# Kernel optimization log

Measured on AMD Instinct MI355X. Metric: run time of the kernel, lower is better.

Reference implementation:

```python
import jax, jax.numpy as jnp
import numpy as np

EPS = 1e-5
B, NPB, G = 8, 12500, 64
N = B * NPB
N_EMB, NI, NF = 256, 128, 64
C = NI // 2  # 64


def _bn_relu(x, g, b):
    m = jnp.mean(x, axis=0)
    v = jnp.mean((x - m) ** 2, axis=0)
    return jax.nn.relu(g * (x - m) * jax.lax.rsqrt(v + EPS) + b)


def setup_inputs() -> dict:
    rng = np.random.default_rng(0)
    # unique voxel coords per batch in a 64^3 grid
    coords = np.concatenate([
        np.stack(np.unravel_index(rng.choice(G ** 3, NPB, replace=False), (G, G, G)), axis=1)
        for _ in range(B)
    ], axis=0).astype(np.int64)  # [N,3]
    batch_idx = np.repeat(np.arange(B), NPB).astype(np.int64)
    keys = ((batch_idx * G + coords[:, 0]) * G + coords[:, 1]) * G + coords[:, 2]
    order = np.argsort(keys)
    skeys = keys[order]
    offs = np.array([[dx, dy, dz] for dx in (-1, 0, 1) for dy in (-1, 0, 1) for dz in (-1, 0, 1)], np.int64)
    nbr = np.full((27, N), -1, np.int32)  # rulebook: input idx feeding each output per offset
    for k in range(27):
        nc = coords + offs[k]
        inb = np.all((nc >= 0) & (nc < G), axis=1)
        q = ((batch_idx * G + nc[:, 0]) * G + nc[:, 1]) * G + nc[:, 2]
        pos = np.clip(np.searchsorted(skeys, q), 0, N - 1)
        hit = inb & (skeys[pos] == q)
        nbr[k] = np.where(hit, order[pos], -1).astype(np.int32)

    key = jax.random.key(0)
    ks = jax.random.split(key, 8)
    s1 = 1.0 / np.sqrt(NI)
    s3 = 1.0 / np.sqrt(27 * C)
    su = 1.0 / np.sqrt(C)
    st = 1.0 / np.sqrt(N_EMB)
    return {
        "feats": jax.random.normal(ks[0], (N, NI), jnp.float32),
        "t": jax.random.normal(ks[1], (B, N_EMB), jnp.float32),
        "w_fuse": jax.random.normal(ks[2], (NI, C), jnp.float32) * s1,
        "g1": jnp.ones((C,), jnp.float32), "b1": jnp.zeros((C,), jnp.float32),
        "w_temb": jax.random.normal(ks[3], (N_EMB, C), jnp.float32) * st,
        "b_temb": jnp.zeros((C,), jnp.float32),
        "w3": jax.random.normal(ks[4], (27, C, C), jnp.float32) * s3,
        "g2": jnp.ones((C,), jnp.float32), "b2": jnp.zeros((C,), jnp.float32),
        "wup": jax.random.normal(ks[5], (8, C, NF), jnp.float32) * su,
        "g3": jnp.ones((NF,), jnp.float32), "b3": jnp.zeros((NF,), jnp.float32),
        "batch_idx": jnp.asarray(batch_idx, jnp.int32),
        "nbr": jnp.asarray(nbr),
    }


def reference(feats, t, w_fuse, g1, b1, w_temb, b_temb, w3, g2, b2, wup, g3, b3, batch_idx, nbr):
    # feature_fusion: 1x1 sparse conv == per-point GEMM, then BN + ReLU
    h = _bn_relu(feats @ w_fuse, g1, b1)  # [N, C]
    # time embedding injected per point via batch index
    emb = jax.nn.silu(t) @ w_temb + b_temb  # [B, C]
    h = h + emb[batch_idx]
    # 3x3x3 submanifold sparse conv: gather-GEMM-scatter per kernel offset
    n = h.shape[0]
    out = jnp.zeros_like(h)
    for k in range(nbr.shape[0]):  # fixed 27 offsets
        idx = nbr[k]
        valid = (idx >= 0)[:, None]
        g_k = jnp.where(valid, h[jnp.clip(idx, 0, n - 1)], 0.0)
        out = out + g_k @ w3[k]
    h2 = _bn_relu(out, g2, b2)  # [N, C]
    # transposed conv k=2 s=2: each input spawns 8 unique children -> per-offset GEMM
    up = jnp.einsum('nc,kcf->nkf', h2, wup).reshape(n * wup.shape[0], wup.shape[2])  # [8N, NF]
    return _bn_relu(up, g3, b3)
```

## Files before the change

### kernel.cpp

```cpp
#include <hip/hip_runtime.h>

#define EPSV 1e-5f

typedef __attribute__((ext_vector_type(8))) short short8;
typedef __attribute__((ext_vector_type(4))) short s16x4;
typedef __attribute__((ext_vector_type(4))) float f32x4;
typedef unsigned short ushort_t;

__device__ inline ushort_t f2bf(float f) {
    unsigned int x = __builtin_bit_cast(unsigned int, f);
    unsigned int r = (x + 0x7fffu + ((x >> 16) & 1u)) >> 16;
    return (ushort_t)r;
}
__device__ inline float bf2f(ushort_t u) {
    return __builtin_bit_cast(float, (unsigned int)u << 16);
}

__global__ __launch_bounds__(256) void k_prep(
    const float* __restrict__ w_fuse, const float* __restrict__ w3,
    const float* __restrict__ wup,
    const float* __restrict__ tin, const float* __restrict__ w_temb,
    const float* __restrict__ b_temb, float* __restrict__ emb,
    ushort_t* __restrict__ wfuset2, ushort_t* __restrict__ w3t2,
    ushort_t* __restrict__ wupt, ushort_t* __restrict__ wupt2) {
    if (blockIdx.x == 720) {
        __shared__ float st[8 * 256];
        int t = threadIdx.x;
        for (int i = t; i < 2048; i += 256) { float v = tin[i]; st[i] = v / (1.f + __expf(-v)); }
        __syncthreads();
        for (int p = t; p < 512; p += 256) {
            int bb = p >> 6, c = p & 63;
            float acc = b_temb[c];
            for (int e = 0; e < 256; e++) acc += st[bb * 256 + e] * w_temb[e * 64 + c];
            emb[bb * 64 + c] = acc;
        }
        return;
    }
    int i = blockIdx.x * 256 + threadIdx.x;
    if (i < 8192) {
        int kk = i & 127, ln = (i >> 7) & 15, j = i >> 11;
        wfuset2[i] = f2bf(w_fuse[kk * 64 + 4 * ln + j]);
    } else if (i < 118784) {
        int p = i - 8192;
        int kk = p & 63, ln = (p >> 6) & 15, j = (p >> 10) & 3, k = p >> 12;
        w3t2[p] = f2bf(w3[k * 4096 + kk * 64 + 4 * ln + j]);
    } else if (i < 151552) {
        int p = i - 118784;
        int uk = p >> 12, r = p & 4095, f = r >> 6, c = r & 63;
        wupt[p] = f2bf(wup[uk * 4096 + c * 64 + f]);
    } else if (i < 184320) {
        int p = i - 151552;
        int kk = p & 63, ln = (p >> 6) & 15, j = (p >> 10) & 3, uk = p >> 12;
        wupt2[p] = f2bf(wup[uk * 4096 + kk * 64 + 4 * ln + j]);
    }
}

__global__ __launch_bounds__(256) void k_gemm_fuse(
    const float* __restrict__ feats, const ushort_t* __restrict__ wfuset2,
    ushort_t* __restrict__ T, float* __restrict__ partialT, int npts) {
    __shared__ float sm[4][128];
    int t = threadIdx.x, bid = blockIdx.x;
    int lane = t & 63, w = t >> 6, q = lane >> 4, ln = lane & 15;
    int rbase = bid * 64 + w * 16;
    int row = rbase + ln;
    bool rv = row < npts;
    short8 afr[4];
#pragma unroll
    for (int s = 0; s < 4; s++) {
        short8 v = (short8)0;
        if (rv) {
            const float* src = feats + (size_t)row * 128 + s * 32 + q * 8;
            float4 a = *(const float4*)src;
            float4 b = *(const float4*)(src + 4);
            ushort_t u[8] = {f2bf(a.x), f2bf(a.y), f2bf(a.z), f2bf(a.w),
                             f2bf(b.x), f2bf(b.y), f2bf(b.z), f2bf(b.w)};
            v = *(short8*)u;
        }
        afr[s] = v;
    }
    f32x4 acc[4];
#pragma unroll
    for (int j = 0; j < 4; j++) acc[j] = (f32x4)0.f;
#pragma unroll
    for (int s = 0; s < 4; s++)
#pragma unroll
        for (int j = 0; j < 4; j++) {
            short8 bfr = *(const short8*)&wfuset2[j * 2048 + ln * 128 + s * 32 + q * 8];
            acc[j] = __builtin_amdgcn_mfma_f32_16x16x32_bf16(afr[s], bfr, acc[j], 0, 0, 0);
        }
    float ps[4] = {0, 0, 0, 0}, pq[4] = {0, 0, 0, 0};
#pragma unroll
    for (int r = 0; r < 4; r++) {
        int rr = rbase + q * 4 + r;
        ushort_t o[4];
#pragma unroll
        for (int j = 0; j < 4; j++) {
            float v = acc[j][r];
            ps[j] += v; pq[j] += v * v;
            o[j] = f2bf(v);
        }
        if (rr < npts) *(s16x4*)&T[(size_t)rr * 64 + 4 * ln] = *(s16x4*)o;
    }
#pragma unroll
    for (int j = 0; j < 4; j++) {
        ps[j] += __shfl_xor(ps[j], 16); ps[j] += __shfl_xor(ps[j], 32);
        pq[j] += __shfl_xor(pq[j], 16); pq[j] += __shfl_xor(pq[j], 32);
    }
    if (lane < 16) {
#pragma unroll
        for (int j = 0; j < 4; j++) {
            sm[w][ln * 4 + j] = ps[j];
            sm[w][64 + ln * 4 + j] = pq[j];
        }
    }
    __syncthreads();
    if (t < 128)
        partialT[(size_t)t * 2048 + bid] = sm[0][t] + sm[1][t] + sm[2][t] + sm[3][t];
}

__global__ __launch_bounds__(256) void k_finalize(
    const float* __restrict__ partialT, int nrows, float inv_count,
    const float* __restrict__ g, const float* __restrict__ b, float* __restrict__ prm) {
    int c = blockIdx.x;
    int t = threadIdx.x;
    float S = 0.f, Q = 0.f;
    for (int r = t; r < nrows; r += 256) {
        S += partialT[(size_t)c * 2048 + r];
        Q += partialT[(size_t)(64 + c) * 2048 + r];
    }
#pragma unroll
    for (int d = 1; d < 64; d <<= 1) { S += __shfl_xor(S, d); Q += __shfl_xor(Q, d); }
    __shared__ float sS[4], sQ[4];
    int w = t >> 6;
    if ((t & 63) == 0) { sS[w] = S; sQ[w] = Q; }
    __syncthreads();
    if (t == 0) {
        float s = sS[0] + sS[1] + sS[2] + sS[3];
        float qq = sQ[0] + sQ[1] + sQ[2] + sQ[3];
        float mean = s * inv_count;
        float var = qq * inv_count - mean * mean;
        float scale = g[c] * rsqrtf(var + EPSV);
        prm[c] = scale;
        prm[64 + c] = b[c] - mean * scale;
    }
}

__global__ __launch_bounds__(256) void k_apply1(
    const ushort_t* __restrict__ T, const float* __restrict__ prm,
    const float* __restrict__ emb, const int* __restrict__ bidx,
    ushort_t* __restrict__ h, int npts) {
    int tid = blockIdx.x * 256 + threadIdx.x;
    if (tid >= npts * 8) return;
    int row = tid >> 3, c0 = (tid & 7) * 8;
    int bi = bidx[row];
    short8 x = *(const short8*)&T[(size_t)row * 64 + c0];
    ushort_t o[8];
#pragma unroll
    for (int j = 0; j < 8; j++) {
        int c = c0 + j;
        float v = prm[c] * bf2f((ushort_t)x[j]) + prm[64 + c];
        v = fmaxf(v, 0.f) + emb[bi * 64 + c];
        o[j] = f2bf(v);
    }
    *(short8*)&h[(size_t)row * 64 + c0] = *(short8*)o;
}

__global__ __launch_bounds__(512, 2) void k_conv27(
    const ushort_t* __restrict__ h, const ushort_t* __restrict__ w3t2,
    const int* __restrict__ nbr,
    ushort_t* __restrict__ out2, float* __restrict__ partialT, int npts) {
    __shared__ ushort_t Bl[2][4 * 4096];
    __shared__ float sm[8][128];
    int nwg = gridDim.x;
    int qc = nwg >> 3, rm = nwg & 7;
    int xcd = blockIdx.x & 7, pos = blockIdx.x >> 3;
    int bid = (xcd < rm ? xcd * (qc + 1) : rm * (qc + 1) + (xcd - rm) * qc) + pos;
    int t = threadIdx.x;
    int lane = t & 63, w = t >> 6, q = lane >> 4, ln = lane & 15;
    int rbase = bid * 256 + w * 32;
    int row0 = rbase + ln, row1 = rbase + 16 + ln;
    bool rv0 = row0 < npts, rv1 = row1 < npts;
    int D = t * 16;
    int blk = D >> 10, lane_d = (D >> 4) & 63;
    int srcByte = (blk >> 1) * 2048 + (lane_d & 15) * 128 + (blk & 1) * 64 + (lane_d >> 4) * 16;
    const char* wsrc = (const char*)w3t2 + srcByte;
    char* lbase0 = (char*)&Bl[0][0] + (size_t)w * 1024;
    char* lbase1 = (char*)&Bl[1][0] + (size_t)w * 1024;
#define STAGE(kk, slot, bufp) \
    __builtin_amdgcn_global_load_lds((const unsigned int*)(wsrc + (size_t)(kk) * 8192), \
                                     (unsigned int*)((bufp) + (size_t)(slot) * 8192), 16, 0, 0)
    STAGE(0, 0, lbase0); STAGE(1, 1, lbase0); STAGE(2, 2, lbase0); STAGE(3, 3, lbase0);
    f32x4 acc[2][4];
#pragma unroll
    for (int g = 0; g < 2; g++)
#pragma unroll
        for (int j = 0; j < 4; j++) acc[g][j] = (f32x4)0.f;
    __syncthreads();
#pragma unroll
    for (int c = 0; c < 7; c++) {
        const int nk = (c == 6) ? 3 : 4;
        int id0[4], id1[4];
#pragma unroll
        for (int r = 0; r < 4; r++)
            if (r < nk) {
                int kk = c * 4 + r;
                id0[r] = rv0 ? nbr[(size_t)kk * npts + row0] : -1;
                id1[r] = rv1 ? nbr[(size_t)kk * npts + row1] : -1;
            }
        if (c < 6) {
            const int nkn = (c == 5) ? 3 : 4;
            char* nb = ((c + 1) & 1) ? lbase1 : lbase0;
#pragma unroll
            for (int r = 0; r < 4; r++)
                if (r < nkn) STAGE(4 * (c + 1) + r, r, nb);
        }
        const ushort_t* bl = (c & 1) ? &Bl[1][0] : &Bl[0][0];
#pragma unroll
        for (int r = 0; r < 4; r++) {
            if (r < nk) {
                bool any0 = __any(id0[r] >= 0), any1 = __any(id1[r] >= 0);
                if (any0 || any1) {
                    short8 a00 = (short8)0, a01 = (short8)0;
                    short8 a10 = (short8)0, a11 = (short8)0;
                    if (id0[r] >= 0) {
                        const ushort_t* hp0 = h + (size_t)id0[r] * 64 + q * 8;
                        a00 = *(const short8*)hp0;
                        a01 = *(const short8*)(hp0 + 32);
                    }
                    if (id1[r] >= 0) {
                        const ushort_t* hp1 = h + (size_t)id1[r] * 64 + q * 8;
                        a10 = *(const short8*)hp1;
                        a11 = *(const short8*)(hp1 + 32);
                    }
                    const ushort_t* bt = bl + r * 4096;
#pragma unroll
                    for (int j = 0; j < 4; j++) {
                        short8 b0 = *(const short8*)&bt[(j * 2 + 0) * 512 + lane * 8];
                        short8 b1 = *(const short8*)&bt[(j * 2 + 1) * 512 + lane * 8];
                        if (any0) {
                            acc[0][j] = __builtin_amdgcn_mfma_f32_16x16x32_bf16(a00, b0, acc[0][j], 0, 0, 0);
                            acc[0][j] = __builtin_amdgcn_mfma_f32_16x16x32_bf16(a01, b1, acc[0][j], 0, 0, 0);
                        }
                        if (any1) {
                            acc[1][j] = __builtin_amdgcn_mfma_f32_16x16x32_bf16(a10, b0, acc[1][j], 0, 0, 0);
                            acc[1][j] = __builtin_amdgcn_mfma_f32_16x16x32_bf16(a11, b1, acc[1][j], 0, 0, 0);
                        }
                    }
                }
            }
        }
        __syncthreads();
    }
#undef STAGE
    float ps[4] = {0, 0, 0, 0}, pq[4] = {0, 0, 0, 0};
#pragma unroll
    for (int g = 0; g < 2; g++)
#pragma unroll
        for (int r = 0; r < 4; r++) {
            int rr = rbase + g * 16 + q * 4 + r;
            ushort_t o[4];
#pragma unroll
            for (int j = 0; j < 4; j++) {
                float v = acc[g][j][r];
                ps[j] += v; pq[j] += v * v;
                o[j] = f2bf(v);
            }
            if (rr < npts) *(s16x4*)&out2[(size_t)rr * 64 + 4 * ln] = *(s16x4*)o;
        }
#pragma unroll
    for (int j = 0; j < 4; j++) {
        ps[j] += __shfl_xor(ps[j], 16); ps[j] += __shfl_xor(ps[j], 32);
        pq[j] += __shfl_xor(pq[j], 16); pq[j] += __shfl_xor(pq[j], 32);
    }
    if (lane < 16) {
#pragma unroll
        for (int j = 0; j < 4; j++) {
            sm[w][ln * 4 + j] = ps[j];
            sm[w][64 + ln * 4 + j] = pq[j];
        }
    }
    __syncthreads();
    if (t < 128) {
        float s = 0.f;
#pragma unroll
        for (int i = 0; i < 8; i++) s += sm[i][t];
        partialT[(size_t)t * 2048 + bid] = s;
    }
}

__global__ __launch_bounds__(256) void k_apply2up(
    const ushort_t* __restrict__ out2, const float* __restrict__ prm2,
    const ushort_t* __restrict__ wupt,
    float* __restrict__ partialT, int npts) {
    __shared__ ushort_t A[64 * 72];
    int t = threadIdx.x, bid = blockIdx.x;
    int lane = t & 63, w = t >> 6, q = lane >> 4, ln = lane & 15;
    int nbase = bid * 64;
    for (int i2 = 0; i2 < 2; i2++) {
        int slot = i2 * 256 + t;
        int row = slot >> 3, seg = slot & 7;
        int n = nbase + row;
        short8 val = (short8)0;
        if (n < npts) {
            short8 x = *(const short8*)&out2[(size_t)n * 64 + seg * 8];
            ushort_t o[8];
#pragma unroll
            for (int j = 0; j < 8; j++) {
                int c = seg * 8 + j;
                float v = prm2[c] * bf2f((ushort_t)x[j]) + prm2[64 + c];
                o[j] = f2bf(fmaxf(v, 0.f));
            }
            val = *(short8*)o;
        }
        *(short8*)&A[row * 72 + seg * 8] = val;
    }
    __syncthreads();
    int col = w * 16 + ln;
    short8 afr[4][2];
    for (int i = 0; i < 4; i++)
        for (int s = 0; s < 2; s++)
            afr[i][s] = *(const short8*)&A[(i * 16 + ln) * 72 + s * 32 + q * 8];
    float ps = 0.f, pq = 0.f;
    for (int uk = 0; uk < 8; uk++) {
        f32x4 acc[4];
        for (int i = 0; i < 4; i++) acc[i] = (f32x4)0.f;
        for (int s = 0; s < 2; s++) {
            short8 bfr = *(const short8*)&wupt[(size_t)uk * 4096 + col * 64 + s * 32 + q * 8];
            for (int i = 0; i < 4; i++)
                acc[i] = __builtin_amdgcn_mfma_f32_16x16x32_bf16(afr[i][s], bfr, acc[i], 0, 0, 0);
        }
        for (int i = 0; i < 4; i++)
            for (int r = 0; r < 4; r++) { float v = acc[i][r]; ps += v; pq += v * v; }
    }
    ps += __shfl_xor(ps, 16); ps += __shfl_xor(ps, 32);
    pq += __shfl_xor(pq, 16); pq += __shfl_xor(pq, 32);
    if (lane < 16) {
        partialT[(size_t)col * 2048 + bid] = ps;
        partialT[(size_t)(64 + col) * 2048 + bid] = pq;
    }
}

__global__ __launch_bounds__(512) void k_up(
    const ushort_t* __restrict__ out2, const ushort_t* __restrict__ wupt2,
    const float* __restrict__ prm2, const float* __restrict__ prm3,
    float* __restrict__ outp, int npts) {
    int t = threadIdx.x, bid = blockIdx.x;
    int lane = t & 63, w = t >> 6, q = lane >> 4, ln = lane & 15;
    int rbase = bid * 256 + w * 32;
    short8 afr[2][2];
#pragma unroll
    for (int g = 0; g < 2; g++) {
        int row = rbase + g * 16 + ln;
#pragma unroll
        for (int s = 0; s < 2; s++) {
            short8 v = (short8)0;
            if (row < npts) {
                short8 x = *(const short8*)&out2[(size_t)row * 64 + s * 32 + q * 8];
                ushort_t o[8];
#pragma unroll
                for (int j = 0; j < 8; j++) {
                    int c = s * 32 + q * 8 + j;
                    float vv = prm2[c] * bf2f((ushort_t)x[j]) + prm2[64 + c];
                    o[j] = f2bf(fmaxf(vv, 0.f));
                }
                v = *(short8*)o;
            }
            afr[g][s] = v;
        }
    }
    float4 sc = *(const float4*)&prm3[4 * ln];
    float4 sh = *(const float4*)&prm3[64 + 4 * ln];
    for (int uk = 0; uk < 8; uk++) {
        short8 bfr[2][4];
#pragma unroll
        for (int s = 0; s < 2; s++)
#pragma unroll
            for (int j = 0; j < 4; j++)
                bfr[s][j] = *(const short8*)&wupt2[(size_t)uk * 4096 + j * 1024 + ln * 64 + s * 32 + q * 8];
#pragma unroll
        for (int g = 0; g < 2; g++) {
            f32x4 acc[4];
#pragma unroll
            for (int j = 0; j < 4; j++) acc[j] = (f32x4)0.f;
#pragma unroll
            for (int s = 0; s < 2; s++)
#pragma unroll
                for (int j = 0; j < 4; j++)
                    acc[j] = __builtin_amdgcn_mfma_f32_16x16x32_bf16(afr[g][s], bfr[s][j], acc[j], 0, 0, 0);
#pragma unroll
            for (int r = 0; r < 4; r++) {
                int rr = rbase + g * 16 + q * 4 + r;
                if (rr < npts) {
                    f32x4 y;
                    y[0] = fmaxf(sc.x * acc[0][r] + sh.x, 0.f);
                    y[1] = fmaxf(sc.y * acc[1][r] + sh.y, 0.f);
                    y[2] = fmaxf(sc.z * acc[2][r] + sh.z, 0.f);
                    y[3] = fmaxf(sc.w * acc[3][r] + sh.w, 0.f);
                    __builtin_nontemporal_store(y, (f32x4*)&outp[((size_t)rr * 8 + uk) * 64 + 4 * ln]);
                }
            }
        }
    }
}

extern "C" void kernel_launch(void* const* d_in, const int* in_sizes, int n_in,
                              void* d_out, int out_size, void* d_ws, size_t ws_size,
                              hipStream_t stream) {
    const float* feats  = (const float*)d_in[0];
    const float* tin    = (const float*)d_in[1];
    const float* w_fuse = (const float*)d_in[2];
    const float* g1     = (const float*)d_in[3];
    const float* b1     = (const float*)d_in[4];
    const float* w_temb = (const float*)d_in[5];
    const float* b_temb = (const float*)d_in[6];
    const float* w3     = (const float*)d_in[7];
    const float* g2     = (const float*)d_in[8];
    const float* b2     = (const float*)d_in[9];
    const float* wup    = (const float*)d_in[10];
    const float* g3     = (const float*)d_in[11];
    const float* b3     = (const float*)d_in[12];
    const int* bidx     = (const int*)d_in[13];
    const int* nbr      = (const int*)d_in[14];

    int npts = in_sizes[13];
    float* dout = (float*)d_out;

    char* ob = (char*)d_out;
    ushort_t* T = (ushort_t*)ob;
    ushort_t* h = (ushort_t*)(ob + (size_t)npts * 128);

    char* ws = (char*)d_ws;
    float* partialT   = (float*)ws;
    float* prm        = (float*)(ws + 1048576);
    float* emb        = (float*)(ws + 1048576 + 4096);
    ushort_t* wfuset2 = (ushort_t*)(ws + 1048576 + 8192);
    ushort_t* w3t2    = (ushort_t*)(ws + 1048576 + 8192 + 16384);
    ushort_t* wupt    = (ushort_t*)(ws + 1048576 + 8192 + 16384 + 221184);
    ushort_t* wupt2   = (ushort_t*)(ws + 1048576 + 8192 + 16384 + 221184 + 65536);
    ushort_t* out2    = (ushort_t*)(ws + 1048576 + 8192 + 16384 + 221184 + 131072);

    int nblk  = (npts + 63) / 64;
    int nblk3 = (npts + 255) / 256;
    int napp  = (npts * 8 + 255) / 256;

    k_prep<<<721, 256, 0, stream>>>(w_fuse, w3, wup, tin, w_temb, b_temb, emb,
                                    wfuset2, w3t2, wupt, wupt2);
    k_gemm_fuse<<<nblk, 256, 0, stream>>>(feats, wfuset2, T, partialT, npts);
    k_finalize<<<64, 256, 0, stream>>>(partialT, nblk, 1.f / npts, g1, b1, prm);
    k_apply1<<<napp, 256, 0, stream>>>(T, prm, emb, bidx, h, npts);
    k_conv27<<<nblk3, 512, 0, stream>>>(h, w3t2, nbr, out2, partialT, npts);
    k_finalize<<<64, 256, 0, stream>>>(partialT, nblk3, 1.f / npts, g2, b2, prm + 128);
    k_apply2up<<<nblk, 256, 0, stream>>>(out2, prm + 128, wupt, partialT, npts);
    k_finalize<<<64, 256, 0, stream>>>(partialT, nblk, 1.f / (8.f * npts), g3, b3, prm + 256);
    k_up<<<nblk3, 512, 0, stream>>>(out2, wupt2, prm + 128, prm + 256, dout, npts);
}
```

Before: 159.2 us.

## Transpose rulebook per point and prefetch next-offset neighbor gathers in conv27

Adds a kernel that transposes the neighbor rulebook into a per-point, 32-entry padded layout, so conv27 can load four offsets' indices with one int4 load. The conv loop now software-pipelines the irregular row gathers: it fetches the h rows for offset k+1 while running the MFMAs for offset k, and loads index groups one chunk ahead. The aim is to hide gather latency behind compute. The cost is an extra transpose pass over about 12.8MB of indices, more live registers, and nbrT stored in the output buffer beyond the h region.

```diff
diff --git a/kernel.cpp b/kernel.cpp
--- a/kernel.cpp
+++ b/kernel.cpp
@@ -14,6 +14,9 @@
 }
 __device__ inline float bf2f(ushort_t u) {
     return __builtin_bit_cast(float, (unsigned int)u << 16);
+}
+__device__ inline int elem4(int4 v, int r) {
+    return r == 0 ? v.x : r == 1 ? v.y : r == 2 ? v.z : v.w;
 }
 
 __global__ __launch_bounds__(256) void k_prep(
@@ -55,6 +58,14 @@
     }
 }
 
+__global__ __launch_bounds__(256) void k_nbrT(
+    const int* __restrict__ nbr, int* __restrict__ nbrT, int npts) {
+    int tid = blockIdx.x * 256 + threadIdx.x;
+    if (tid >= npts * 32) return;
+    int row = tid >> 5, k = tid & 31;
+    nbrT[tid] = (k < 27) ? nbr[(size_t)k * npts + row] : -1;
+}
+
 __global__ __launch_bounds__(256) void k_gemm_fuse(
     const float* __restrict__ feats, const ushort_t* __restrict__ wfuset2,
     ushort_t* __restrict__ T, float* __restrict__ partialT, int npts) {
@@ -167,7 +178,7 @@
 
 __global__ __launch_bounds__(512, 2) void k_conv27(
     const ushort_t* __restrict__ h, const ushort_t* __restrict__ w3t2,
-    const int* __restrict__ nbr,
+    const int* __restrict__ nbrT,
     ushort_t* __restrict__ out2, float* __restrict__ partialT, int npts) {
     __shared__ ushort_t Bl[2][4 * 4096];
     __shared__ float sm[8][128];
@@ -189,24 +200,41 @@
 #define STAGE(kk, slot, bufp) \
     __builtin_amdgcn_global_load_lds((const unsigned int*)(wsrc + (size_t)(kk) * 8192), \
                                      (unsigned int*)((bufp) + (size_t)(slot) * 8192), 16, 0, 0)
+    int4 pidx[2][2];
+    short8 pa[2][4];
+#define LOADIDX(bf, cc) do { \
+        pidx[bf][0] = make_int4(-1, -1, -1, -1); \
+        pidx[bf][1] = make_int4(-1, -1, -1, -1); \
+        if (rv0) pidx[bf][0] = *(const int4*)&nbrT[(size_t)row0 * 32 + (cc) * 4]; \
+        if (rv1) pidx[bf][1] = *(const int4*)&nbrT[(size_t)row1 * 32 + (cc) * 4]; \
+    } while (0)
+#define GATHER(kk) do { \
+        const int cb_ = (kk) >> 2, rr_ = (kk) & 3, bf_ = (kk) & 1; \
+        int i0_ = elem4(pidx[cb_ & 1][0], rr_); \
+        int i1_ = elem4(pidx[cb_ & 1][1], rr_); \
+        pa[bf_][0] = (short8)0; pa[bf_][1] = (short8)0; \
+        pa[bf_][2] = (short8)0; pa[bf_][3] = (short8)0; \
+        if (i0_ >= 0) { \
+            const ushort_t* p_ = h + (size_t)i0_ * 64 + q * 8; \
+            pa[bf_][0] = *(const short8*)p_; pa[bf_][1] = *(const short8*)(p_ + 32); \
+        } \
+        if (i1_ >= 0) { \
+            const ushort_t* p_ = h + (size_t)i1_ * 64 + q * 8; \
+            pa[bf_][2] = *(const short8*)p_; pa[bf_][3] = *(const short8*)(p_ + 32); \
+        } \
+    } while (0)
+    f32x4 acc[2][4];
+#pragma unroll
+    for (int g = 0; g < 2; g++)
+#pragma unroll
+        for (int j = 0; j < 4; j++) acc[g][j] = (f32x4)0.f;
+    LOADIDX(0, 0);
     STAGE(0, 0, lbase0); STAGE(1, 1, lbase0); STAGE(2, 2, lbase0); STAGE(3, 3, lbase0);
-    f32x4 acc[2][4];
-#pragma unroll
-    for (int g = 0; g < 2; g++)
-#pragma unroll
-        for (int j = 0; j < 4; j++) acc[g][j] = (f32x4)0.f;
+    GATHER(0);
+    LOADIDX(1, 1);
     __syncthreads();
 #pragma unroll
     for (int c = 0; c < 7; c++) {
-        const int nk = (c == 6) ? 3 : 4;
-        int id0[4], id1[4];
-#pragma unroll
-        for (int r = 0; r < 4; r++)
-            if (r < nk) {
-                int kk = c * 4 + r;
-                id0[r] = rv0 ? nbr[(size_t)kk * npts + row0] : -1;
-                id1[r] = rv1 ? nbr[(size_t)kk * npts + row1] : -1;
-            }
         if (c < 6) {
             const int nkn = (c == 5) ? 3 : 4;
             char* nb = ((c + 1) & 1) ? lbase1 : lbase0;
@@ -214,36 +242,29 @@
             for (int r = 0; r < 4; r++)
                 if (r < nkn) STAGE(4 * (c + 1) + r, r, nb);
         }
-        const ushort_t* bl = (c & 1) ? &Bl[1][0] : &Bl[0][0];
+        if (c >= 1 && c <= 5) LOADIDX((c + 1) & 1, c + 1);
 #pragma unroll
         for (int r = 0; r < 4; r++) {
-            if (r < nk) {
-                bool any0 = __any(id0[r] >= 0), any1 = __any(id1[r] >= 0);
+            const int k = c * 4 + r;
+            if (k < 27) {
+                if (k + 1 <= 26) GATHER(k + 1);
+                int i0 = elem4(pidx[c & 1][0], r);
+                int i1 = elem4(pidx[c & 1][1], r);
+                bool any0 = __any(i0 >= 0), any1 = __any(i1 >= 0);
                 if (any0 || any1) {
-                    short8 a00 = (short8)0, a01 = (short8)0;
-                    short8 a10 = (short8)0, a11 = (short8)0;
-                    if (id0[r] >= 0) {
-                        const ushort_t* hp0 = h + (size_t)id0[r] * 64 + q * 8;
-                        a00 = *(const short8*)hp0;
-                        a01 = *(const short8*)(hp0 + 32);
-                    }
-                    if (id1[r] >= 0) {
-                        const ushort_t* hp1 = h + (size_t)id1[r] * 64 + q * 8;
-                        a10 = *(const short8*)hp1;
-                        a11 = *(const short8*)(hp1 + 32);
-                    }
-                    const ushort_t* bt = bl + r * 4096;
+                    const int bf = k & 1;
+                    const ushort_t* bt = ((c & 1) ? &Bl[1][0] : &Bl[0][0]) + r * 4096;
 #pragma unroll
                     for (int j = 0; j < 4; j++) {
                         short8 b0 = *(const short8*)&bt[(j * 2 + 0) * 512 + lane * 8];
                         short8 b1 = *(const short8*)&bt[(j * 2 + 1) * 512 + lane * 8];
                         if (any0) {
-                            acc[0][j] = __builtin_amdgcn_mfma_f32_16x16x32_bf16(a00, b0, acc[0][j], 0, 0, 0);
-                            acc[0][j] = __builtin_amdgcn_mfma_f32_16x16x32_bf16(a01, b1, acc[0][j], 0, 0, 0);
+                            acc[0][j] = __builtin_amdgcn_mfma_f32_16x16x32_bf16(pa[bf][0], b0, acc[0][j], 0, 0, 0);
+                            acc[0][j] = __builtin_amdgcn_mfma_f32_16x16x32_bf16(pa[bf][1], b1, acc[0][j], 0, 0, 0);
                         }
                         if (any1) {
-                            acc[1][j] = __builtin_amdgcn_mfma_f32_16x16x32_bf16(a10, b0, acc[1][j], 0, 0, 0);
-                            acc[1][j] = __builtin_amdgcn_mfma_f32_16x16x32_bf16(a11, b1, acc[1][j], 0, 0, 0);
+                            acc[1][j] = __builtin_amdgcn_mfma_f32_16x16x32_bf16(pa[bf][2], b0, acc[1][j], 0, 0, 0);
+                            acc[1][j] = __builtin_amdgcn_mfma_f32_16x16x32_bf16(pa[bf][3], b1, acc[1][j], 0, 0, 0);
                         }
                     }
                 }
@@ -252,6 +273,8 @@
         __syncthreads();
     }
 #undef STAGE
+#undef LOADIDX
+#undef GATHER
     float ps[4] = {0, 0, 0, 0}, pq[4] = {0, 0, 0, 0};
 #pragma unroll
     for (int g = 0; g < 2; g++)
@@ -426,8 +449,9 @@
     float* dout = (float*)d_out;
 
     char* ob = (char*)d_out;
-    ushort_t* T = (ushort_t*)ob;
-    ushort_t* h = (ushort_t*)(ob + (size_t)npts * 128);
+    ushort_t* T  = (ushort_t*)ob;
+    ushort_t* h  = (ushort_t*)(ob + (size_t)npts * 128);
+    int* nbrT    = (int*)(ob + (size_t)npts * 256);
 
     char* ws = (char*)d_ws;
     float* partialT   = (float*)ws;
@@ -442,13 +466,15 @@
     int nblk  = (npts + 63) / 64;
     int nblk3 = (npts + 255) / 256;
     int napp  = (npts * 8 + 255) / 256;
+    int ntr   = (npts * 32 + 255) / 256;
 
     k_prep<<<721, 256, 0, stream>>>(w_fuse, w3, wup, tin, w_temb, b_temb, emb,
                                     wfuset2, w3t2, wupt, wupt2);
+    k_nbrT<<<ntr, 256, 0, stream>>>(nbr, nbrT, npts);
     k_gemm_fuse<<<nblk, 256, 0, stream>>>(feats, wfuset2, T, partialT, npts);
     k_finalize<<<64, 256, 0, stream>>>(partialT, nblk, 1.f / npts, g1, b1, prm);
     k_apply1<<<napp, 256, 0, stream>>>(T, prm, emb, bidx, h, npts);
-    k_conv27<<<nblk3, 512, 0, stream>>>(h, w3t2, nbr, out2, partialT, npts);
+    k_conv27<<<nblk3, 512, 0, stream>>>(h, w3t2, nbrT, out2, partialT, npts);
     k_finalize<<<64, 256, 0, stream>>>(partialT, nblk3, 1.f / npts, g2, b2, prm + 128);
     k_apply2up<<<nblk, 256, 0, stream>>>(out2, prm + 128, wupt, partialT, npts);
     k_finalize<<<64, 256, 0, stream>>>(partialT, nblk, 1.f / (8.f * npts), g3, b3, prm + 256);
```

New measurement: 173.5 us. 1.09x slower.
